# Kernel tuning notes

Measured on AMD Instinct MI355X. Metric: run time of the kernel, lower is better.

The kernel has to match this reference:

```python
import jax, jax.numpy as jnp
import numpy as np

BATCH, C_IN, H = 16, 32, 224
N_FILT, K = 64, 5


def setup_inputs() -> dict:
    key = jax.random.key(0)
    k1, k2 = jax.random.split(key)
    x = jax.random.normal(k1, (BATCH, C_IN, H, H), dtype=jnp.float32)
    weight = jax.random.normal(k2, (N_FILT, C_IN, K, K), dtype=jnp.float32)
    bias = jnp.zeros((N_FILT,), dtype=jnp.float32)  # torch init: zeros(1) per filter
    return {"x": x, "weight": weight, "bias": bias}


def reference(x, weight, bias):
    # Fully-connected conv layer: stride 1, VALID padding.
    # Equivalent to stacking per-filter sum(x_patch * w) + scalar bias.
    out = jax.lax.conv_general_dilated(
        x, weight,
        window_strides=(1, 1),
        padding='VALID',
        dimension_numbers=('NCHW', 'OIHW', 'NCHW'),
    )
    # per-filter scalar bias broadcast over spatial dims
    return out + bias[None, :, None, None]
```

## Files before the change

kernel.cpp:

```cpp
#include <hip/hip_runtime.h>

#define CI    32
#define IH    224
#define IW    224
#define OHS   220
#define OWS   220
#define NF    64
#define KS    5

#define XCOLS 228
#define CP    36
#define WPD   40
#define XROWS 8
#define NBUFW (KS * NF * WPD)

#define RCHKF 912
#define ROWBF (RCHKF * 16)
#define SROWSF 8
#define TCHKF (RCHKF * SROWSF)

typedef __attribute__((ext_vector_type(4))) float   f32x4;
typedef __attribute__((ext_vector_type(4))) __bf16  bf16x4;
typedef __attribute__((ext_vector_type(8))) __bf16  bf16x8;

__global__ __launch_bounds__(256)
void prep_kernel(const float* __restrict__ x, const float* __restrict__ w,
                 __bf16* __restrict__ xh, __bf16* __restrict__ wp) {
  int chunk = blockIdx.x * 256 + threadIdx.x;
  int c8  = (chunk & 3) * 8;
  int pos = chunk >> 2;
  int ww  = pos % IW;
  int nh  = pos / IW;
  int n   = nh / IH;
  int h   = nh - n * IH;
  const float* xp = x + ((size_t)n * CI + c8) * (IH * IW) + h * IW + ww;
  bf16x8 v;
#pragma unroll
  for (int j = 0; j < 8; ++j) v[j] = (__bf16)xp[(size_t)j * (IH * IW)];
  *(bf16x8*)(xh + (size_t)pos * CI + c8) = v;

  if (blockIdx.x < 200) {
    int i = blockIdx.x * 256 + threadIdx.x;
    int c   = i & (CI - 1);
    int f   = (i >> 5) & (NF - 1);
    int tap = i >> 11;
    int kh = tap / KS, kw = tap % KS;
    wp[i] = (__bf16)w[((f * CI + c) * KS + kh) * KS + kw];
  }
}

__global__ __launch_bounds__(512, 2)
void conv_full(const __bf16* __restrict__ xh, const __bf16* __restrict__ wp,
               const float* __restrict__ bias, float* __restrict__ out) {
  __shared__ __bf16 xs[TCHKF * 8];

  const int tid  = threadIdx.x;
  const int lane = tid & 63;
  const int wv   = tid >> 6;
  const int m    = lane & 15;
  const int q    = lane >> 4;

  const int bid = blockIdx.x;
  const int lid = (bid & 7) * 110 + (bid >> 3);
  const int n   = lid / 55;
  const int oh0 = (lid - n * 55) * 4;

  {
    const __bf16* xb = xh + (size_t)(n * IH + oh0) * (IW * CI);
    for (int g = wv; g < TCHKF / 64; g += 8) {
      int L = g * 64 + lane;
      int r = L / RCHKF;
      int c = L - r * RCHKF;
      __builtin_amdgcn_global_load_lds(
          (const __attribute__((address_space(1))) void*)(xb + (size_t)r * (IW * CI) + c * 8),
          (__attribute__((address_space(3))) void*)&xs[g * 512], 16, 0, 0);
    }
  }

  int cbj[7], rjv[7], bbase[7];
#pragma unroll
  for (int j = 0; j < 7; ++j) {
    int t  = wv + j * 8;
    int rj = t / 14;
    rjv[j] = rj;
    cbj[j] = (t % 14) * 16;
    bbase[j] = rj * ROWBF + (cbj[j] + m) * 64 + q * 16;
  }

  f32x4 acc[28];
#pragma unroll
  for (int i = 0; i < 28; ++i) { f32x4 z = {0.f, 0.f, 0.f, 0.f}; acc[i] = z; }

  const __bf16* wpl = wp + m * CI + q * 8;

  __syncthreads();

  for (int kh = 0; kh < KS; ++kh) {
    const int khb = kh * ROWBF;
#pragma unroll
    for (int kw = 0; kw < KS; ++kw) {
      bf16x8 af[4];
#pragma unroll
      for (int ft = 0; ft < 4; ++ft)
        af[ft] = *(const bf16x8*)(wpl + (size_t)(kh * KS + kw) * (NF * CI) + ft * 16 * CI);
#pragma unroll
      for (int j = 0; j < 7; ++j) {
        bf16x8 bv = *(const bf16x8*)((const char*)xs + khb + bbase[j] + kw * 64);
#pragma unroll
        for (int ft = 0; ft < 4; ++ft)
          acc[j * 4 + ft] =
              __builtin_amdgcn_mfma_f32_16x16x32_bf16(af[ft], bv, acc[j * 4 + ft], 0, 0, 0);
      }
    }
  }

  float bvv[16];
#pragma unroll
  for (int ft = 0; ft < 4; ++ft)
#pragma unroll
    for (int rg = 0; rg < 4; ++rg)
      bvv[ft * 4 + rg] = bias[ft * 16 + q * 4 + rg];

#pragma unroll
  for (int j = 0; j < 7; ++j) {
    int ow = cbj[j] + m;
    if (ow < OWS) {
      int oh = oh0 + rjv[j];
#pragma unroll
      for (int ft = 0; ft < 4; ++ft)
#pragma unroll
        for (int rg = 0; rg < 4; ++rg) {
          int f = ft * 16 + q * 4 + rg;
          out[(((size_t)n * NF + f) * OHS + oh) * OWS + ow] =
              acc[j * 4 + ft][rg] + bvv[ft * 4 + rg];
        }
    }
  }
}

__global__ void repack_w_kernel(const float* __restrict__ w, __bf16* __restrict__ wp) {
  int i = blockIdx.x * 256 + threadIdx.x;
  if (i >= KS * KS * NF * CI) return;
  int c   = i & (CI - 1);
  int f   = (i >> 5) & (NF - 1);
  int tap = i >> 11;
  int kh = tap / KS, kw = tap % KS;
  wp[i] = (__bf16)w[((f * CI + c) * KS + kh) * KS + kw];
}

template <bool USE_WS>
__global__ __launch_bounds__(512, 1)
void conv_main(const float* __restrict__ x, const float* __restrict__ w,
               const __bf16* __restrict__ wp, const float* __restrict__ bias,
               float* __restrict__ out) {
  __shared__ __bf16 xs[XROWS * XCOLS * CP];
  __shared__ __bf16 wsm[NBUFW];

  const int tid  = threadIdx.x;
  const int lane = tid & 63;
  const int wv   = tid >> 6;
  const int m    = lane & 15;
  const int q    = lane >> 4;

  int bid = blockIdx.x;
  int lid = (bid >> 3) + (bid & 7) * 110;
  const int n   = lid / 55;
  const int oh0 = (lid % 55) * 4;

  {
    const float* xn = x + (size_t)n * CI * IH * IW;
    for (int p = tid; p < XROWS * 56 * 8; p += 512) {
      int pc   = p & 7;
      int pg   = p >> 3;
      int pcol = pg % 56;
      int prow = pg / 56;
      int row  = oh0 + prow;
      f32x4 v0 = *(const f32x4*)(xn + ((size_t)(pc * 4 + 0) * IH + row) * IW + pcol * 4);
      f32x4 v1 = *(const f32x4*)(xn + ((size_t)(pc * 4 + 1) * IH + row) * IW + pcol * 4);
      f32x4 v2 = *(const f32x4*)(xn + ((size_t)(pc * 4 + 2) * IH + row) * IW + pcol * 4);
      f32x4 v3 = *(const f32x4*)(xn + ((size_t)(pc * 4 + 3) * IH + row) * IW + pcol * 4);
#pragma unroll
      for (int dcol = 0; dcol < 4; ++dcol) {
        bf16x4 t;
        t[0] = (__bf16)v0[dcol]; t[1] = (__bf16)v1[dcol];
        t[2] = (__bf16)v2[dcol]; t[3] = (__bf16)v3[dcol];
        *(bf16x4*)&xs[(prow * XCOLS + pcol * 4 + dcol) * CP + pc * 4] = t;
      }
    }
    for (int z = tid; z < XROWS * 4 * CP; z += 512) {
      int rr  = z / (4 * CP);
      int rem = z - rr * (4 * CP);
      xs[(rr * XCOLS + 224) * CP + rem] = (__bf16)0.0f;
    }
  }

  if (USE_WS) {
    for (int i = tid; i < NF * CI * KS / 8; i += 512) {
      int c0 = (i & 3) * 8;
      int f  = (i >> 2) & 63;
      int kw = i >> 8;
      bf16x8 v = *(const bf16x8*)(wp + ((size_t)(0 * KS + kw) * NF + f) * CI + c0);
      *(bf16x8*)&wsm[(kw * NF + f) * WPD + c0] = v;
    }
  } else {
    for (int i = tid; i < KS * NF * CI; i += 512) {
      int c  = i & 31;
      int f  = (i >> 5) & 63;
      int kw = i >> 11;
      wsm[(kw * NF + f) * WPD + c] = (__bf16)w[((f * CI + c) * KS + 0) * KS + kw];
    }
  }
  __syncthreads();

  int rj[7], cbj[7], xoff[7];
#pragma unroll
  for (int j = 0; j < 7; ++j) {
    int t   = wv + j * 8;
    rj[j]   = t / 14;
    cbj[j]  = (t % 14) * 16;
    xoff[j] = (rj[j] * XCOLS + cbj[j] + m) * CP + q * 8;
  }

  f32x4 acc[28];
#pragma unroll
  for (int i = 0; i < 28; ++i) { f32x4 z = {0.f, 0.f, 0.f, 0.f}; acc[i] = z; }

  for (int kh = 0; kh < KS; ++kh) {
    bf16x8 pw[3];
    if (USE_WS && kh < KS - 1) {
#pragma unroll
      for (int it = 0; it < 3; ++it) {
        int e = it * 512 + tid;
        if (e < 1280) {
          int c0 = (e & 3) * 8;
          int f  = (e >> 2) & 63;
          int kw = e >> 8;
          pw[it] = *(const bf16x8*)(wp + ((size_t)((kh + 1) * KS + kw) * NF + f) * CI + c0);
        }
      }
    }

#pragma unroll
    for (int kw = 0; kw < KS; ++kw) {
      bf16x8 af[4];
#pragma unroll
      for (int ft = 0; ft < 4; ++ft)
        af[ft] = *(const bf16x8*)&wsm[(kw * NF + ft * 16 + m) * WPD + q * 8];
#pragma unroll
      for (int j = 0; j < 7; ++j) {
        const __bf16* bp = &xs[xoff[j] + (kh * XCOLS + kw) * CP];
        bf16x4 lo = *(const bf16x4*)bp;
        bf16x4 hi = *(const bf16x4*)(bp + 4);
        bf16x8 bv8 = __builtin_shufflevector(lo, hi, 0, 1, 2, 3, 4, 5, 6, 7);
#pragma unroll
        for (int ft = 0; ft < 4; ++ft)
          acc[j * 4 + ft] =
              __builtin_amdgcn_mfma_f32_16x16x32_bf16(af[ft], bv8, acc[j * 4 + ft], 0, 0, 0);
      }
    }

    if (kh < KS - 1) {
      __syncthreads();
      if (USE_WS) {
#pragma unroll
        for (int it = 0; it < 3; ++it) {
          int e = it * 512 + tid;
          if (e < 1280) {
            int c0 = (e & 3) * 8;
            int f  = (e >> 2) & 63;
            int kw = e >> 8;
            *(bf16x8*)&wsm[(kw * NF + f) * WPD + c0] = pw[it];
          }
        }
      } else {
        for (int i = tid; i < KS * NF * CI; i += 512) {
          int c  = i & 31;
          int f  = (i >> 5) & 63;
          int kw = i >> 11;
          wsm[(kw * NF + f) * WPD + c] =
              (__bf16)w[((f * CI + c) * KS + (kh + 1)) * KS + kw];
        }
      }
      __syncthreads();
    }
  }

  float bvv[16];
#pragma unroll
  for (int ft = 0; ft < 4; ++ft)
#pragma unroll
    for (int rg = 0; rg < 4; ++rg)
      bvv[ft * 4 + rg] = bias[ft * 16 + q * 4 + rg];

#pragma unroll
  for (int j = 0; j < 7; ++j) {
    int ow = cbj[j] + m;
    if (ow < OWS) {
      int oh = oh0 + rj[j];
#pragma unroll
      for (int ft = 0; ft < 4; ++ft) {
#pragma unroll
        for (int rg = 0; rg < 4; ++rg) {
          int f = ft * 16 + q * 4 + rg;
          out[(((size_t)n * NF + f) * OHS + oh) * OWS + ow] = acc[j * 4 + ft][rg] + bvv[ft * 4 + rg];
        }
      }
    }
  }
}

extern "C" void kernel_launch(void* const* d_in, const int* in_sizes, int n_in,
                              void* d_out, int out_size, void* d_ws, size_t ws_size,
                              hipStream_t stream) {
  const float* x    = (const float*)d_in[0];
  const float* w    = (const float*)d_in[1];
  const float* bias = (const float*)d_in[2];
  float* out = (float*)d_out;

  const int    NW = KS * KS * NF * CI;
  const size_t WB = (size_t)NW * sizeof(__bf16);
  const size_t XB = (size_t)16 * IH * IW * CI * sizeof(__bf16);

  if (ws_size >= XB + WB) {
    __bf16* xhp = (__bf16*)d_ws;
    __bf16* wp  = (__bf16*)((char*)d_ws + XB);
    prep_kernel<<<(16 * IH * IW * 4) / 256, 256, 0, stream>>>(x, w, xhp, wp);
    conv_full<<<880, 512, 0, stream>>>(xhp, wp, bias, out);
  } else if (ws_size >= WB) {
    __bf16* wp = (__bf16*)d_ws;
    repack_w_kernel<<<(NW + 255) / 256, 256, 0, stream>>>(w, wp);
    conv_main<true><<<880, 512, 0, stream>>>(x, w, wp, bias, out);
  } else {
    conv_main<false><<<880, 512, 0, stream>>>(x, w, nullptr, bias, out);
  }
}
```

Before: 395.9 us.

## Stream input rows through a three-slot LDS ring with smaller blocks

Replaces the kernel that stages all eight input rows into LDS before computing with a version where each 256-thread block computes two output rows. Input rows stream through a three-slot LDS ring, and the next row's asynchronous global-to-LDS copy is issued while the current kernel row is being computed. This cuts the LDS footprint so more blocks can reside per CU, and it overlaps loads with MFMA work. The cost is more redundant input-row loads per output row (6 rows for 2 outputs instead of 8 for 4) and a barrier per kernel row.

```diff
diff --git a/kernel.cpp b/kernel.cpp
--- a/kernel.cpp
+++ b/kernel.cpp
@@ -14,10 +14,10 @@
 #define XROWS 8
 #define NBUFW (KS * NF * WPD)
 
-#define RCHKF 912
-#define ROWBF (RCHKF * 16)
-#define SROWSF 8
-#define TCHKF (RCHKF * SROWSF)
+#define RCHKR 912
+#define ROWBR (RCHKR * 16)
+#define ROWER (RCHKR * 8)
+#define NSLOT 3
 
 typedef __attribute__((ext_vector_type(4))) float   f32x4;
 typedef __attribute__((ext_vector_type(4))) __bf16  bf16x4;
@@ -49,10 +49,25 @@
   }
 }
 
-__global__ __launch_bounds__(512, 2)
-void conv_full(const __bf16* __restrict__ xh, const __bf16* __restrict__ wp,
-               const float* __restrict__ bias, float* __restrict__ out) {
-  __shared__ __bf16 xs[TCHKF * 8];
+__device__ __forceinline__ void stage_row(const __bf16* __restrict__ src,
+                                          __bf16* dst, int wv, int lane) {
+#pragma unroll
+  for (int g = 0; g < 14; ++g) {
+    if ((g & 3) == wv)
+      __builtin_amdgcn_global_load_lds(
+          (const __attribute__((address_space(1))) void*)(src + g * 512 + lane * 8),
+          (__attribute__((address_space(3))) void*)(dst + g * 512), 16, 0, 0);
+  }
+  if (wv == 3 && lane < 16)
+    __builtin_amdgcn_global_load_lds(
+        (const __attribute__((address_space(1))) void*)(src + 14 * 512 + lane * 8),
+        (__attribute__((address_space(3))) void*)(dst + 14 * 512), 16, 0, 0);
+}
+
+__global__ __launch_bounds__(256, 3)
+void conv_ring2(const __bf16* __restrict__ xh, const __bf16* __restrict__ wp,
+                const float* __restrict__ bias, float* __restrict__ out) {
+  __shared__ __bf16 xs[NSLOT * ROWER];
 
   const int tid  = threadIdx.x;
   const int lane = tid & 63;
@@ -61,30 +76,25 @@
   const int q    = lane >> 4;
 
   const int bid = blockIdx.x;
-  const int lid = (bid & 7) * 110 + (bid >> 3);
-  const int n   = lid / 55;
-  const int oh0 = (lid - n * 55) * 4;
-
-  {
-    const __bf16* xb = xh + (size_t)(n * IH + oh0) * (IW * CI);
-    for (int g = wv; g < TCHKF / 64; g += 8) {
-      int L = g * 64 + lane;
-      int r = L / RCHKF;
-      int c = L - r * RCHKF;
-      __builtin_amdgcn_global_load_lds(
-          (const __attribute__((address_space(1))) void*)(xb + (size_t)r * (IW * CI) + c * 8),
-          (__attribute__((address_space(3))) void*)&xs[g * 512], 16, 0, 0);
-    }
-  }
-
-  int cbj[7], rjv[7], bbase[7];
+  const int lid = (bid & 7) * 220 + (bid >> 3);
+  const int n   = lid / 110;
+  const int oh0 = (lid - n * 110) * 2;
+
+  const __bf16* xb = xh + (size_t)(n * IH + oh0) * (IW * CI);
+
+  stage_row(xb,                 xs,             wv, lane);
+  stage_row(xb + (IW * CI),     xs + ROWER,     wv, lane);
+  stage_row(xb + 2 * (IW * CI), xs + 2 * ROWER, wv, lane);
+
+  int cbj[7], boff[7];
+  bool rj1[7];
 #pragma unroll
   for (int j = 0; j < 7; ++j) {
-    int t  = wv + j * 8;
+    int t  = wv + j * 4;
     int rj = t / 14;
-    rjv[j] = rj;
+    rj1[j] = (rj != 0);
     cbj[j] = (t % 14) * 16;
-    bbase[j] = rj * ROWBF + (cbj[j] + m) * 64 + q * 16;
+    boff[j] = (cbj[j] + m) * 64 + q * 16;
   }
 
   f32x4 acc[28];
@@ -95,8 +105,20 @@
 
   __syncthreads();
 
+#pragma unroll
   for (int kh = 0; kh < KS; ++kh) {
-    const int khb = kh * ROWBF;
+    if (kh) {
+      __syncthreads();
+      if (kh <= 3)
+        stage_row(xb + (size_t)(kh + 2) * (IW * CI),
+                  xs + ((kh + 2) % NSLOT) * ROWER, wv, lane);
+    }
+    const int b0 = (kh % NSLOT) * ROWBR;
+    const int b1 = ((kh + 1) % NSLOT) * ROWBR;
+    int sbj[7];
+#pragma unroll
+    for (int j = 0; j < 7; ++j) sbj[j] = (rj1[j] ? b1 : b0) + boff[j];
+
 #pragma unroll
     for (int kw = 0; kw < KS; ++kw) {
       bf16x8 af[4];
@@ -105,7 +127,7 @@
         af[ft] = *(const bf16x8*)(wpl + (size_t)(kh * KS + kw) * (NF * CI) + ft * 16 * CI);
 #pragma unroll
       for (int j = 0; j < 7; ++j) {
-        bf16x8 bv = *(const bf16x8*)((const char*)xs + khb + bbase[j] + kw * 64);
+        bf16x8 bv = *(const bf16x8*)((const char*)xs + sbj[j] + kw * 64);
 #pragma unroll
         for (int ft = 0; ft < 4; ++ft)
           acc[j * 4 + ft] =
@@ -125,7 +147,7 @@
   for (int j = 0; j < 7; ++j) {
     int ow = cbj[j] + m;
     if (ow < OWS) {
-      int oh = oh0 + rjv[j];
+      int oh = oh0 + (rj1[j] ? 1 : 0);
 #pragma unroll
       for (int ft = 0; ft < 4; ++ft)
 #pragma unroll
@@ -325,7 +347,7 @@
     __bf16* xhp = (__bf16*)d_ws;
     __bf16* wp  = (__bf16*)((char*)d_ws + XB);
     prep_kernel<<<(16 * IH * IW * 4) / 256, 256, 0, stream>>>(x, w, xhp, wp);
-    conv_full<<<880, 512, 0, stream>>>(xhp, wp, bias, out);
+    conv_ring2<<<1760, 256, 0, stream>>>(xhp, wp, bias, out);
   } else if (ws_size >= WB) {
     __bf16* wp = (__bf16*)d_ws;
     repack_w_kernel<<<(NW + 255) / 256, 256, 0, stream>>>(w, wp);
```

After: 383.0 us. 1.03x faster.

## Split conv tile into three horizontal bands with smaller 256-thread blocks

Applied to the files above, without the earlier changes.

The main conv kernel now splits each 4-row output strip into three 80-pixel column bands. Each block has 256 threads (4 waves) and loads only an 84-pixel-wide halo into LDS, so it uses about a third of the shared memory. Launch bounds change to allow three blocks per CU, and the grid grows to 2640 blocks, aiming for better occupancy and load balance. The cost is redundant halo loads at band edges, more weight fetches per output, and wasted work in the last band, since 3×80 exceeds 220 columns.

```diff
diff --git a/kernel.cpp b/kernel.cpp
--- a/kernel.cpp
+++ b/kernel.cpp
@@ -14,10 +14,11 @@
 #define XROWS 8
 #define NBUFW (KS * NF * WPD)
 
-#define RCHKF 912
-#define ROWBF (RCHKF * 16)
-#define SROWSF 8
-#define TCHKF (RCHKF * SROWSF)
+#define BPX   80
+#define SPX   84
+#define SCHK  (SPX * 4)
+#define SROWB (SCHK * 16)
+#define NRW   8
 
 typedef __attribute__((ext_vector_type(4))) float   f32x4;
 typedef __attribute__((ext_vector_type(4))) __bf16  bf16x4;
@@ -49,10 +50,10 @@
   }
 }
 
-__global__ __launch_bounds__(512, 2)
-void conv_full(const __bf16* __restrict__ xh, const __bf16* __restrict__ wp,
-               const float* __restrict__ bias, float* __restrict__ out) {
-  __shared__ __bf16 xs[TCHKF * 8];
+__global__ __launch_bounds__(256, 3)
+void conv_t5(const __bf16* __restrict__ xh, const __bf16* __restrict__ wp,
+             const float* __restrict__ bias, float* __restrict__ out) {
+  __shared__ __bf16 xs[NRW * SCHK * 8];
 
   const int tid  = threadIdx.x;
   const int lane = tid & 63;
@@ -60,43 +61,47 @@
   const int m    = lane & 15;
   const int q    = lane >> 4;
 
-  const int bid = blockIdx.x;
-  const int lid = (bid & 7) * 110 + (bid >> 3);
-  const int n   = lid / 55;
-  const int oh0 = (lid - n * 55) * 4;
+  const int bid  = blockIdx.x;
+  const int lid  = (bid & 7) * 330 + (bid >> 3);
+  const int n    = lid / 165;
+  const int rem  = lid - n * 165;
+  const int band = rem % 3;
+  const int oh0  = (rem / 3) * 4;
+  const int px0  = band * BPX;
 
   {
-    const __bf16* xb = xh + (size_t)(n * IH + oh0) * (IW * CI);
-    for (int g = wv; g < TCHKF / 64; g += 8) {
-      int L = g * 64 + lane;
-      int r = L / RCHKF;
-      int c = L - r * RCHKF;
-      __builtin_amdgcn_global_load_lds(
-          (const __attribute__((address_space(1))) void*)(xb + (size_t)r * (IW * CI) + c * 8),
-          (__attribute__((address_space(3))) void*)&xs[g * 512], 16, 0, 0);
-    }
-  }
-
-  int cbj[7], rjv[7], bbase[7];
-#pragma unroll
-  for (int j = 0; j < 7; ++j) {
-    int t  = wv + j * 8;
-    int rj = t / 14;
-    rjv[j] = rj;
-    cbj[j] = (t % 14) * 16;
-    bbase[j] = rj * ROWBF + (cbj[j] + m) * 64 + q * 16;
-  }
-
-  f32x4 acc[28];
-#pragma unroll
-  for (int i = 0; i < 28; ++i) { f32x4 z = {0.f, 0.f, 0.f, 0.f}; acc[i] = z; }
+    const __bf16* xb = xh + (((size_t)n * IH + oh0) * IW + px0) * CI;
+    for (int u = wv; u < 48; u += 4) {
+      int r = u / 6;
+      int k = u - r * 6;
+      int c = k * 64 + lane;
+      if (k < 5 || lane < 16)
+        __builtin_amdgcn_global_load_lds(
+            (const __attribute__((address_space(1))) void*)(xb + (size_t)r * (IW * CI) + c * 8),
+            (__attribute__((address_space(3))) void*)&xs[(r * SCHK + k * 64) * 8], 16, 0, 0);
+    }
+  }
+
+  int bbase[5];
+#pragma unroll
+  for (int j = 0; j < 5; ++j) {
+    int t  = wv + j * 4;
+    int rj = t / 5;
+    int ct = t - rj * 5;
+    bbase[j] = rj * SROWB + ((ct * 16 + m) * 4 + q) * 16;
+  }
+
+  f32x4 acc[20];
+#pragma unroll
+  for (int i = 0; i < 20; ++i) { f32x4 z = {0.f, 0.f, 0.f, 0.f}; acc[i] = z; }
 
   const __bf16* wpl = wp + m * CI + q * 8;
 
   __syncthreads();
 
+#pragma unroll
   for (int kh = 0; kh < KS; ++kh) {
-    const int khb = kh * ROWBF;
+    const int khb = kh * SROWB;
 #pragma unroll
     for (int kw = 0; kw < KS; ++kw) {
       bf16x8 af[4];
@@ -104,7 +109,7 @@
       for (int ft = 0; ft < 4; ++ft)
         af[ft] = *(const bf16x8*)(wpl + (size_t)(kh * KS + kw) * (NF * CI) + ft * 16 * CI);
 #pragma unroll
-      for (int j = 0; j < 7; ++j) {
+      for (int j = 0; j < 5; ++j) {
         bf16x8 bv = *(const bf16x8*)((const char*)xs + khb + bbase[j] + kw * 64);
 #pragma unroll
         for (int ft = 0; ft < 4; ++ft)
@@ -122,10 +127,13 @@
       bvv[ft * 4 + rg] = bias[ft * 16 + q * 4 + rg];
 
 #pragma unroll
-  for (int j = 0; j < 7; ++j) {
-    int ow = cbj[j] + m;
+  for (int j = 0; j < 5; ++j) {
+    int t  = wv + j * 4;
+    int rj = t / 5;
+    int ct = t - rj * 5;
+    int ow = px0 + ct * 16 + m;
     if (ow < OWS) {
-      int oh = oh0 + rjv[j];
+      int oh = oh0 + rj;
 #pragma unroll
       for (int ft = 0; ft < 4; ++ft)
 #pragma unroll
@@ -325,7 +333,7 @@
     __bf16* xhp = (__bf16*)d_ws;
     __bf16* wp  = (__bf16*)((char*)d_ws + XB);
     prep_kernel<<<(16 * IH * IW * 4) / 256, 256, 0, stream>>>(x, w, xhp, wp);
-    conv_full<<<880, 512, 0, stream>>>(xhp, wp, bias, out);
+    conv_t5<<<2640, 256, 0, stream>>>(xhp, wp, bias, out);
   } else if (ws_size >= WB) {
     __bf16* wp = (__bf16*)d_ws;
     repack_w_kernel<<<(NW + 255) / 256, 256, 0, stream>>>(w, wp);
```

Measured after the change: 383.6 us. 3.1% less time.
